# Optimization experiments

Measured on AMD Instinct MI355X. Metric: run time of the kernel, lower is better.

Reference implementation:

```python
import jax, jax.numpy as jnp
import numpy as np

D_MODEL = 768
NUM_HEADS = 12
D_K = D_MODEL // NUM_HEADS


def setup_inputs() -> dict:
    key = jax.random.key(0)
    ks = jax.random.split(key, 7)
    B, S = 4, 2048
    query = jax.random.normal(ks[0], (B, S, D_MODEL), dtype=jnp.float32)
    key_t = jax.random.normal(ks[1], (B, S, D_MODEL), dtype=jnp.float32)
    value = jax.random.normal(ks[2], (B, S, D_MODEL), dtype=jnp.float32)
    lim = 1.0 / np.sqrt(D_MODEL)
    Wq = jax.random.uniform(ks[3], (D_MODEL, D_MODEL), jnp.float32, -lim, lim)  # torch Linear weight [out,in]
    bq = jax.random.uniform(ks[4], (D_MODEL,), jnp.float32, -lim, lim)
    Wo = jax.random.uniform(ks[5], (D_MODEL, D_MODEL), jnp.float32, -lim, lim)
    bo = jax.random.uniform(ks[6], (D_MODEL,), jnp.float32, -lim, lim)
    return {"query": query, "key": key_t, "value": value,
            "Wq": Wq, "bq": bq, "Wo": Wo, "bo": bo}


def _proj_heads(x, W, b):
    # x: [B,S,D] -> [B,H,S,d_k]; torch Linear: x @ W.T + b
    B, S, _ = x.shape
    y = x @ W.T + b
    return y.reshape(B, S, NUM_HEADS, D_K).transpose(0, 2, 1, 3)


def reference(query, key, value, Wq, bq, Wo, bo):
    # Faithful to source: linear_q is used for q, k AND v (source bug).
    q = _proj_heads(query, Wq, bq)
    k = _proj_heads(key, Wq, bq)
    v = _proj_heads(value, Wq, bq)
    scale = 1.0 / jnp.sqrt(jnp.asarray(D_K, q.dtype))
    scores = jnp.einsum('bhqd,bhkd->bhqk', q, k) * scale  # [B,H,S,S]
    attn = jax.nn.softmax(scores, axis=-1)
    out = jnp.einsum('bhqk,bhkd->bhqd', attn, v)  # [B,H,S,d_k]
    B, H, S, dk = out.shape
    out = out.transpose(0, 2, 1, 3).reshape(B, S, H * dk)
    return out @ Wo.T + bo
```

## Files before the change

### kernel.cpp

```cpp
#include <hip/hip_runtime.h>
#include <math.h>

typedef _Float16 f16x8 __attribute__((ext_vector_type(8)));
typedef _Float16 f16x4 __attribute__((ext_vector_type(4)));
typedef float    f32x4 __attribute__((ext_vector_type(4)));
typedef unsigned short us4 __attribute__((ext_vector_type(4)));

constexpr int DM = 768, NH = 12, DK = 64, SEQ = 2048, BB = 4;
constexpr int MROWS = BB * SEQ;
constexpr size_t XELE = (size_t)MROWS * DM;
constexpr size_t WELE = (size_t)DM * DM;

constexpr size_t OFF_X16  = 0;
constexpr size_t OFF_W16  = 3 * XELE;
constexpr size_t OFF_WO16 = OFF_W16 + WELE;
constexpr size_t OFF_QKV  = OFF_WO16 + WELE;
constexpr size_t OFF_ATT  = OFF_QKV + 3 * XELE;
constexpr size_t TOT_CVT  = OFF_QKV;


constexpr float QSCALE = 0.125f * 1.44269504f;

__device__ __forceinline__ void gload16(const _Float16* g, _Float16* l) {
    __builtin_amdgcn_global_load_lds(
        (const __attribute__((address_space(1))) unsigned int*)g,
        (__attribute__((address_space(3))) unsigned int*)l, 16, 0, 0);
}

__global__ __launch_bounds__(256) void cvt_kernel(
    const float* __restrict__ q, const float* __restrict__ k,
    const float* __restrict__ v, const float* __restrict__ wq,
    const float* __restrict__ wo, _Float16* __restrict__ dst)
{
    const size_t i = ((size_t)blockIdx.x * 256 + threadIdx.x) * 4;
    if (i >= TOT_CVT) return;
    const float* src; size_t base;
    if      (i < XELE)            { src = q;  base = 0; }
    else if (i < 2 * XELE)        { src = k;  base = XELE; }
    else if (i < 3 * XELE)        { src = v;  base = 2 * XELE; }
    else if (i < OFF_WO16)        { src = wq; base = OFF_W16; }
    else                          { src = wo; base = OFF_WO16; }
    const float4 f = *(const float4*)(src + (i - base));
    _Float16 h4[4] = {(_Float16)f.x, (_Float16)f.y, (_Float16)f.z, (_Float16)f.w};
    *(us4*)(dst + i) = *(us4*)h4;
}

template <int MODE>
__global__ __launch_bounds__(256) void mfma_gemm(
    const _Float16* __restrict__ Xbase, const _Float16* __restrict__ Wmat,
    const float* __restrict__ bias, void* __restrict__ Yout)
{
    __shared__ _Float16 smem[(MODE == 0) ? 128 * 136 : 8192];
    _Float16* As = smem;
    _Float16* Bs = smem + 4096;

    const int tid  = threadIdx.x;
    const int w    = tid >> 6, lane = tid & 63;
    const int cl   = lane & 15;
    const int g    = lane >> 4;
    const int m0   = blockIdx.y * 128, n0 = blockIdx.x * 128;
    const int z    = blockIdx.z;
    const _Float16* X = Xbase + (size_t)z * XELE;

    const int wr = w >> 1, wc = w & 1;
    const int lrow = lane >> 2;
    const int lcol = (lane & 3) * 8;

    f32x4 acc[4][4] = {};

    for (int kk = 0; kk < DM; kk += 32) {
        __syncthreads();
#pragma unroll
        for (int t = 0; t < 2; ++t) {
            const int c = w + t * 4;
            gload16(X + (size_t)(m0 + c * 16 + lrow) * DM + kk + lcol,
                    &As[c * 512]);
            gload16(Wmat + (size_t)(n0 + c * 16 + lrow) * DM + kk + lcol,
                    &Bs[c * 512]);
        }
        __syncthreads();

        f16x8 a[4], bfr[4];
#pragma unroll
        for (int mt = 0; mt < 4; ++mt)
            a[mt] = *(const f16x8*)&As[(wr * 64 + mt * 16 + cl) * 32 + g * 8];
#pragma unroll
        for (int nt = 0; nt < 4; ++nt)
            bfr[nt] = *(const f16x8*)&Bs[(wc * 64 + nt * 16 + cl) * 32 + g * 8];
#pragma unroll
        for (int mt = 0; mt < 4; ++mt)
#pragma unroll
            for (int nt = 0; nt < 4; ++nt)
                acc[mt][nt] = __builtin_amdgcn_mfma_f32_16x16x32_f16(
                    a[mt], bfr[nt], acc[mt][nt], 0, 0, 0);
    }

    if (MODE == 1) {
#pragma unroll
        for (int nt = 0; nt < 4; ++nt) {
            const int col = n0 + wc * 64 + nt * 16 + cl;
            const float bv = bias[col];
#pragma unroll
            for (int mt = 0; mt < 4; ++mt)
#pragma unroll
                for (int r = 0; r < 4; ++r) {
                    const int row = m0 + wr * 64 + mt * 16 + g * 4 + r;
                    ((float*)Yout)[(size_t)row * DM + col] = acc[mt][nt][r] + bv;
                }
        }
        return;
    }

    __syncthreads();
    const float sc = (z == 0) ? QSCALE : 1.0f;
#pragma unroll
    for (int nt = 0; nt < 4; ++nt) {
        const int col = wc * 64 + nt * 16 + cl;
        const float bv = bias[n0 + col];
#pragma unroll
        for (int mt = 0; mt < 4; ++mt)
#pragma unroll
            for (int r = 0; r < 4; ++r) {
                const int row = wr * 64 + mt * 16 + g * 4 + r;
                const _Float16 hv = (_Float16)((acc[mt][nt][r] + bv) * sc);
                if (z == 2) smem[col * 136 + row] = hv;
                else        smem[row * 136 + col] = hv;
            }
    }
    __syncthreads();

    _Float16* Yz = (_Float16*)Yout + (size_t)z * XELE;
#pragma unroll
    for (int it = 0; it < 8; ++it) {
        const int idx = tid + it * 256;
        const int row = idx >> 4;
        const int grp = idx & 15;
        const f16x8 vv = *(const f16x8*)&smem[row * 136 + grp * 8];
        if (z == 2) {
            const int f  = n0 + row, hh = f >> 6, d = f & 63;
            const int gm = m0 + grp * 8;
            const int bb = gm >> 11, s = gm & (SEQ - 1);
            const int ssw = (s & ~63) | ((((s >> 3) & 7) ^ (d & 7)) << 3);
            *(f16x8*)&Yz[(((size_t)bb * NH + hh) * DK + d) * SEQ + ssw] = vv;
        } else {
            const int gm = m0 + row;
            const int bb = gm >> 11, s = gm & (SEQ - 1);
            const int n  = n0 + grp * 8, hh = n >> 6, d0 = n & 63;
            const int dsw = ((((d0 >> 3) ^ (s & 7)) & 7) << 3);
            *(f16x8*)&Yz[(((size_t)bb * NH + hh) * SEQ + s) * DK + dsw] = vv;
        }
    }
}

__global__ __launch_bounds__(256) void flash3(
    const _Float16* __restrict__ qkv, _Float16* __restrict__ attno)
{
    __shared__ _Float16 Ks[64 * 64];
    __shared__ _Float16 Vt[64 * 64];
    __shared__ _Float16 Ps[128 * 72];

    const int tid = threadIdx.x;
    const int w = tid >> 6, lane = tid & 63;
    const int cl = lane & 15, g = lane >> 4;
    const int swz = cl & 7;
    const int q0 = blockIdx.x * 128;
    const int h  = blockIdx.y, b = blockIdx.z;

    const size_t headoff = ((size_t)b * NH + h) * SEQ * DK;
    const _Float16* Qg = qkv + headoff;
    const _Float16* Kg = qkv + XELE + headoff;
    const _Float16* Vg = qkv + 2 * XELE + headoff;

    f16x8 qf[2][2];
#pragma unroll
    for (int qt = 0; qt < 2; ++qt)
#pragma unroll
        for (int ks = 0; ks < 2; ++ks)
            qf[qt][ks] = *(const f16x8*)(
                Qg + (size_t)(q0 + w * 32 + qt * 16 + cl) * DK
                   + (((ks * 4 + g) ^ swz) << 3));

    float m_run[2] = {-1e30f, -1e30f};
    float l_run[2] = {0.f, 0.f};
    f32x4 acc[2][4] = {};

    for (int j0 = 0; j0 < SEQ; j0 += 64) {
        __syncthreads();
#pragma unroll
        for (int t = 0; t < 2; ++t) {
            const int c = w * 2 + t;
            gload16(Kg + (size_t)(j0 + c * 8 + (lane >> 3)) * DK + (lane & 7) * 8,
                    &Ks[c * 512]);
            gload16(Vg + (size_t)(c * 8 + (lane >> 3)) * SEQ + j0 + (lane & 7) * 8,
                    &Vt[c * 512]);
        }
        __syncthreads();

        f16x8 kf[4][2];
#pragma unroll
        for (int kt = 0; kt < 4; ++kt)
#pragma unroll
            for (int ks = 0; ks < 2; ++ks)
                kf[kt][ks] = *(const f16x8*)&Ks[(kt * 16 + cl) * 64
                                                + (((ks * 4 + g) ^ swz) << 3)];

        f32x4 st[2][4];
#pragma unroll
        for (int qt = 0; qt < 2; ++qt)
#pragma unroll
            for (int kt = 0; kt < 4; ++kt) {
                f32x4 s = {};
#pragma unroll
                for (int ks = 0; ks < 2; ++ks)
                    s = __builtin_amdgcn_mfma_f32_16x16x32_f16(
                        kf[kt][ks], qf[qt][ks], s, 0, 0, 0);
                st[qt][kt] = s;
            }

#pragma unroll
        for (int qt = 0; qt < 2; ++qt) {
            float mx = st[qt][0][0];
#pragma unroll
            for (int kt = 0; kt < 4; ++kt)
#pragma unroll
                for (int r = 0; r < 4; ++r) mx = fmaxf(mx, st[qt][kt][r]);
            mx = fmaxf(mx, __shfl_xor(mx, 16));
            mx = fmaxf(mx, __shfl_xor(mx, 32));
            const float mo = m_run[qt];
            const float mn = fmaxf(mo, mx);
            const float al = __builtin_amdgcn_exp2f(mo - mn);
            m_run[qt] = mn;

            float ps = 0.f;
            const int prow = w * 32 + qt * 16 + cl;
#pragma unroll
            for (int kt = 0; kt < 4; ++kt) {
                float p0 = __builtin_amdgcn_exp2f(st[qt][kt][0] - mn);
                float p1 = __builtin_amdgcn_exp2f(st[qt][kt][1] - mn);
                float p2 = __builtin_amdgcn_exp2f(st[qt][kt][2] - mn);
                float p3 = __builtin_amdgcn_exp2f(st[qt][kt][3] - mn);
                ps += (p0 + p1) + (p2 + p3);
                f16x4 pk = {(_Float16)p0, (_Float16)p1, (_Float16)p2, (_Float16)p3};
                *(f16x4*)&Ps[(size_t)prow * 72 + kt * 16 + g * 4] = pk;
            }
            ps += __shfl_xor(ps, 16);
            ps += __shfl_xor(ps, 32);
            l_run[qt] = l_run[qt] * al + ps;
#pragma unroll
            for (int dt = 0; dt < 4; ++dt)
#pragma unroll
                for (int r = 0; r < 4; ++r) acc[qt][dt][r] *= al;
        }

        f16x8 vf[4][2], pf[2][2];
#pragma unroll
        for (int dt = 0; dt < 4; ++dt)
#pragma unroll
            for (int ks = 0; ks < 2; ++ks)
                vf[dt][ks] = *(const f16x8*)&Vt[(dt * 16 + cl) * 64
                                                + (((ks * 4 + g) ^ swz) << 3)];
#pragma unroll
        for (int qt = 0; qt < 2; ++qt)
#pragma unroll
            for (int ks = 0; ks < 2; ++ks)
                pf[qt][ks] = *(const f16x8*)&Ps[(size_t)(w * 32 + qt * 16 + cl) * 72
                                                + ks * 32 + g * 8];
#pragma unroll
        for (int qt = 0; qt < 2; ++qt)
#pragma unroll
            for (int ks = 0; ks < 2; ++ks)
#pragma unroll
                for (int dt = 0; dt < 4; ++dt)
                    acc[qt][dt] = __builtin_amdgcn_mfma_f32_16x16x32_f16(
                        vf[dt][ks], pf[qt][ks], acc[qt][dt], 0, 0, 0);
    }

#pragma unroll
    for (int qt = 0; qt < 2; ++qt) {
        const float inv = 1.0f / l_run[qt];
        const int q = q0 + w * 32 + qt * 16 + cl;
#pragma unroll
        for (int dt = 0; dt < 4; ++dt) {
            f16x4 pk = {(_Float16)(acc[qt][dt][0] * inv),
                        (_Float16)(acc[qt][dt][1] * inv),
                        (_Float16)(acc[qt][dt][2] * inv),
                        (_Float16)(acc[qt][dt][3] * inv)};
            *(f16x4*)&attno[((size_t)b * SEQ + q) * DM + h * DK + dt * 16 + g * 4] = pk;
        }
    }
}

extern "C" void kernel_launch(void* const* d_in, const int* in_sizes, int n_in,
                              void* d_out, int out_size, void* d_ws, size_t ws_size,
                              hipStream_t stream) {
    const float* q  = (const float*)d_in[0];
    const float* k  = (const float*)d_in[1];
    const float* v  = (const float*)d_in[2];
    const float* Wq = (const float*)d_in[3];
    const float* bq = (const float*)d_in[4];
    const float* Wo = (const float*)d_in[5];
    const float* bo = (const float*)d_in[6];

    _Float16* ws16  = (_Float16*)d_ws;
    _Float16* x16   = ws16 + OFF_X16;
    _Float16* w16   = ws16 + OFF_W16;
    _Float16* wo16  = ws16 + OFF_WO16;
    _Float16* qkv16 = ws16 + OFF_QKV;
    _Float16* att16 = ws16 + OFF_ATT;

    cvt_kernel<<<(int)(TOT_CVT / 1024), 256, 0, stream>>>(q, k, v, Wq, Wo, ws16);

    mfma_gemm<0><<<dim3(DM / 128, MROWS / 128, 3), 256, 0, stream>>>(
        x16, w16, bq, qkv16);

    flash3<<<dim3(SEQ / 128, NH, BB), 256, 0, stream>>>(qkv16, att16);

    mfma_gemm<1><<<dim3(DM / 128, MROWS / 128, 1), 256, 0, stream>>>(
        att16, wo16, bo, (float*)d_out);
}
```

Before: 309.3 us.

## Double-buffer LDS tiles in GEMM and flash attention kernels

Both the projection GEMM and the flash attention kernel now keep two LDS buffers. The next K-slice (GEMM) or K/V tile (attention) is prefetched with async global-to-LDS loads while MFMAs run on the current buffer, which also removes one barrier per iteration. The goal is to hide global-load latency behind compute. In exchange, shared memory per block roughly doubles for those tiles, which may cut occupancy, especially in the attention kernel.

```diff
diff --git a/kernel.cpp b/kernel.cpp
--- a/kernel.cpp
+++ b/kernel.cpp
@@ -50,9 +50,7 @@
     const _Float16* __restrict__ Xbase, const _Float16* __restrict__ Wmat,
     const float* __restrict__ bias, void* __restrict__ Yout)
 {
-    __shared__ _Float16 smem[(MODE == 0) ? 128 * 136 : 8192];
-    _Float16* As = smem;
-    _Float16* Bs = smem + 4096;
+    __shared__ _Float16 smem[(MODE == 0) ? 128 * 136 : 16384];
 
     const int tid  = threadIdx.x;
     const int w    = tid >> 6, lane = tid & 63;
@@ -68,17 +66,29 @@
 
     f32x4 acc[4][4] = {};
 
-    for (int kk = 0; kk < DM; kk += 32) {
+    constexpr int NK = DM / 32;
+#pragma unroll
+    for (int t = 0; t < 2; ++t) {
+        const int c = w + t * 4;
+        gload16(X    + (size_t)(m0 + c * 16 + lrow) * DM + lcol, &smem[c * 512]);
+        gload16(Wmat + (size_t)(n0 + c * 16 + lrow) * DM + lcol, &smem[4096 + c * 512]);
+    }
+
+    int cur = 0;
+    for (int ki = 0; ki < NK; ++ki) {
         __syncthreads();
-#pragma unroll
-        for (int t = 0; t < 2; ++t) {
-            const int c = w + t * 4;
-            gload16(X + (size_t)(m0 + c * 16 + lrow) * DM + kk + lcol,
-                    &As[c * 512]);
-            gload16(Wmat + (size_t)(n0 + c * 16 + lrow) * DM + kk + lcol,
-                    &Bs[c * 512]);
-        }
-        __syncthreads();
+        if (ki + 1 < NK) {
+            const int kn = (ki + 1) * 32;
+            _Float16* dst = &smem[(cur ^ 1) * 8192];
+#pragma unroll
+            for (int t = 0; t < 2; ++t) {
+                const int c = w + t * 4;
+                gload16(X    + (size_t)(m0 + c * 16 + lrow) * DM + kn + lcol, &dst[c * 512]);
+                gload16(Wmat + (size_t)(n0 + c * 16 + lrow) * DM + kn + lcol, &dst[4096 + c * 512]);
+            }
+        }
+        const _Float16* As = &smem[cur * 8192];
+        const _Float16* Bs = As + 4096;
 
         f16x8 a[4], bfr[4];
 #pragma unroll
@@ -93,6 +103,7 @@
             for (int nt = 0; nt < 4; ++nt)
                 acc[mt][nt] = __builtin_amdgcn_mfma_f32_16x16x32_f16(
                     a[mt], bfr[nt], acc[mt][nt], 0, 0, 0);
+        cur ^= 1;
     }
 
     if (MODE == 1) {
@@ -155,8 +166,8 @@
 __global__ __launch_bounds__(256) void flash3(
     const _Float16* __restrict__ qkv, _Float16* __restrict__ attno)
 {
-    __shared__ _Float16 Ks[64 * 64];
-    __shared__ _Float16 Vt[64 * 64];
+    __shared__ _Float16 KsB[2 * 64 * 64];
+    __shared__ _Float16 VtB[2 * 64 * 64];
     __shared__ _Float16 Ps[128 * 72];
 
     const int tid = threadIdx.x;
@@ -171,6 +182,15 @@
     const _Float16* Kg = qkv + XELE + headoff;
     const _Float16* Vg = qkv + 2 * XELE + headoff;
 
+    const int ldr = lane >> 3, ldc = (lane & 7) * 8;
+
+#pragma unroll
+    for (int t = 0; t < 2; ++t) {
+        const int c = w * 2 + t;
+        gload16(Kg + (size_t)(c * 8 + ldr) * DK + ldc, &KsB[c * 512]);
+        gload16(Vg + (size_t)(c * 8 + ldr) * SEQ + ldc, &VtB[c * 512]);
+    }
+
     f16x8 qf[2][2];
 #pragma unroll
     for (int qt = 0; qt < 2; ++qt)
@@ -184,17 +204,22 @@
     float l_run[2] = {0.f, 0.f};
     f32x4 acc[2][4] = {};
 
+    int cur = 0;
     for (int j0 = 0; j0 < SEQ; j0 += 64) {
         __syncthreads();
-#pragma unroll
-        for (int t = 0; t < 2; ++t) {
-            const int c = w * 2 + t;
-            gload16(Kg + (size_t)(j0 + c * 8 + (lane >> 3)) * DK + (lane & 7) * 8,
-                    &Ks[c * 512]);
-            gload16(Vg + (size_t)(c * 8 + (lane >> 3)) * SEQ + j0 + (lane & 7) * 8,
-                    &Vt[c * 512]);
-        }
-        __syncthreads();
+        if (j0 + 64 < SEQ) {
+            const int jn = j0 + 64;
+            _Float16* Kd = &KsB[(cur ^ 1) * 4096];
+            _Float16* Vd = &VtB[(cur ^ 1) * 4096];
+#pragma unroll
+            for (int t = 0; t < 2; ++t) {
+                const int c = w * 2 + t;
+                gload16(Kg + (size_t)(jn + c * 8 + ldr) * DK + ldc, &Kd[c * 512]);
+                gload16(Vg + (size_t)(c * 8 + ldr) * SEQ + jn + ldc, &Vd[c * 512]);
+            }
+        }
+        const _Float16* Ks = &KsB[cur * 4096];
+        const _Float16* Vt = &VtB[cur * 4096];
 
         f16x8 kf[4][2];
 #pragma unroll
@@ -273,6 +298,7 @@
                 for (int dt = 0; dt < 4; ++dt)
                     acc[qt][dt] = __builtin_amdgcn_mfma_f32_16x16x32_f16(
                         vf[dt][ks], pf[qt][ks], acc[qt][dt], 0, 0, 0);
+        cur ^= 1;
     }
 
 #pragma unroll
```

New measurement: 298.6 us. -3.5%, faster.
